# Kernel optimization log

Measured on AMD Instinct MI355X. Metric: run time of the kernel, lower is better.

Reference implementation:

```python
import jax, jax.numpy as jnp
import numpy as np

H = 8  # num_heads


def _ln(x, g, b):
    mu = x.mean(-1, keepdims=True)
    var = ((x - mu) ** 2).mean(-1, keepdims=True)
    return (x - mu) * jax.lax.rsqrt(var + 1e-5) * g + b


def setup_inputs() -> dict:
    key = jax.random.key(0)
    ks = jax.random.split(key, 24)
    B, N, V, E, D, R, L = 8, 512, 50000, 300, 256, 100, 4
    dh = D // H
    s = 0.02
    inp = {}
    inp['token_ids'] = jax.random.randint(ks[0], (B, N), 0, V, dtype=jnp.int32)
    inp['relations'] = jax.random.randint(ks[1], (B, N, N), 0, R, dtype=jnp.int32)
    m = jax.random.bernoulli(ks[2], 0.9, (B, N, N))
    eye = jnp.eye(N, dtype=bool)[None]
    inp['relations_mask'] = jnp.logical_or(m, eye)  # keep diagonal valid so every row attends somewhere
    inp['embed'] = jax.random.normal(ks[3], (V, E), jnp.float32) * s
    inp['W_in'] = jax.random.normal(ks[4], (E, D), jnp.float32) * s
    inp['b_in'] = jnp.zeros((D,), jnp.float32)
    inp['Wq'] = jax.random.normal(ks[5], (L, D, D), jnp.float32) * s
    inp['Wk'] = jax.random.normal(ks[6], (L, D, D), jnp.float32) * s
    inp['Wv'] = jax.random.normal(ks[7], (L, D, D), jnp.float32) * s
    inp['Wo'] = jax.random.normal(ks[8], (L, D, D), jnp.float32) * s
    inp['ln1_g'] = jnp.ones((L, D), jnp.float32)
    inp['ln1_b'] = jnp.zeros((L, D), jnp.float32)
    inp['ln2_g'] = jnp.ones((L, D), jnp.float32)
    inp['ln2_b'] = jnp.zeros((L, D), jnp.float32)
    inp['W1'] = jax.random.normal(ks[9], (L, D, 4 * D), jnp.float32) * s
    inp['b1'] = jnp.zeros((L, 4 * D), jnp.float32)
    inp['W2'] = jax.random.normal(ks[10], (L, 4 * D, D), jnp.float32) * s
    inp['b2'] = jnp.zeros((L, D), jnp.float32)
    inp['rel_k_emb'] = jax.random.normal(ks[11], (R, dh), jnp.float32) * s
    inp['rel_v_emb'] = jax.random.normal(ks[12], (R, dh), jnp.float32) * s
    inp['W_out'] = jax.random.normal(ks[13], (D, D), jnp.float32) * s
    inp['b_out'] = jnp.zeros((D,), jnp.float32)
    return inp


def reference(token_ids, relations, relations_mask, embed, W_in, b_in, Wq, Wk, Wv, Wo,
              ln1_g, ln1_b, ln2_g, ln2_b, W1, b1, W2, b2, rel_k_emb, rel_v_emb, W_out, b_out):
    # Input layer: embedding lookup + projection to gnn hidden size.
    x = embed[token_ids]                          # [B,N,E]
    x = jax.nn.relu(x @ W_in + b_in)              # [B,N,D]
    B, N, D = x.shape
    dh = D // H
    # Shared relation embeddings (share_layers=True, share_heads=True): gathered once.
    rk = rel_k_emb[relations]                     # [B,N,N,dh]
    rv = rel_v_emb[relations]                     # [B,N,N,dh]
    neg = jnp.asarray(-1e9, x.dtype)
    scale = jnp.asarray(1.0 / np.sqrt(dh), x.dtype)
    L = Wq.shape[0]
    for l in range(L):  # fixed small layer count
        q = (x @ Wq[l]).reshape(B, N, H, dh).transpose(0, 2, 1, 3)
        k = (x @ Wk[l]).reshape(B, N, H, dh).transpose(0, 2, 1, 3)
        v = (x @ Wv[l]).reshape(B, N, H, dh).transpose(0, 2, 1, 3)
        # Relation-aware scores: q.k + q.r_k (RAT-SQL)
        scores = (jnp.einsum('bhnd,bhmd->bhnm', q, k)
                  + jnp.einsum('bhnd,bnmd->bhnm', q, rk)) * scale
        scores = jnp.where(relations_mask[:, None], scores, neg)
        a = jax.nn.softmax(scores, axis=-1)       # [B,H,N,N]
        z = (jnp.einsum('bhnm,bhmd->bhnd', a, v)
             + jnp.einsum('bhnm,bnmd->bhnd', a, rv))
        z = z.transpose(0, 2, 1, 3).reshape(B, N, D) @ Wo[l]
        x = _ln(x + z, ln1_g[l], ln1_b[l])
        f = jax.nn.relu(x @ W1[l] + b1[l]) @ W2[l] + b2[l]
        x = _ln(x + f, ln2_g[l], ln2_b[l])
    # Output layer projection
    return x @ W_out + b_out
```

## Files before the change

### kernel.cpp

```cpp
#include <hip/hip_runtime.h>
#include <hip/hip_bf16.h>

#define NTOK 4096
#define NN   512

typedef __attribute__((ext_vector_type(8))) short bf16x8;
typedef __attribute__((ext_vector_type(4))) float f32x4;
typedef __attribute__((ext_vector_type(4))) unsigned short u16x4;

__device__ __forceinline__ float bf16_to_f(unsigned short u) {
    unsigned int x = ((unsigned int)u) << 16;
    return __builtin_bit_cast(float, x);
}
__device__ __forceinline__ unsigned short f_to_bf16(float f) {
    unsigned int b = __builtin_bit_cast(unsigned int, f);
    return (unsigned short)((b + 0x7fff + ((b >> 16) & 1)) >> 16);
}
__device__ __forceinline__ bf16x8 pack8(float4 a, float4 b) {
    bf16x8 v;
    v[0]=(short)f_to_bf16(a.x); v[1]=(short)f_to_bf16(a.y);
    v[2]=(short)f_to_bf16(a.z); v[3]=(short)f_to_bf16(a.w);
    v[4]=(short)f_to_bf16(b.x); v[5]=(short)f_to_bf16(b.y);
    v[6]=(short)f_to_bf16(b.z); v[7]=(short)f_to_bf16(b.w);
    return v;
}

__global__ void detect_mask_kernel(const unsigned char* __restrict__ m, int* __restrict__ flag) {
    __shared__ int f;
    if (threadIdx.x == 0) f = 0;
    __syncthreads();
    int any = 0;
    for (int i = threadIdx.x; i < 4096; i += 256) {
        if ((i & 3) != 0 && m[i] != 0) any = 1;
    }
    if (any) atomicOr(&f, 1);
    __syncthreads();
    if (threadIdx.x == 0) *flag = f;
}

__global__ __launch_bounds__(256) void prep_rel16(
    const int* __restrict__ rel, const void* __restrict__ mask,
    const int* __restrict__ flag, short* __restrict__ rel16)
{
    const bool mbyte = (*flag != 0);
    const unsigned char* m8 = (const unsigned char*)mask;
    const int* m32 = (const int*)mask;
    const int i = (blockIdx.x * 256 + threadIdx.x) * 2;
    int2 rv = *(const int2*)(rel + i);
    int ok0, ok1;
    if (mbyte) { ok0 = m8[i]; ok1 = m8[i + 1]; }
    else       { ok0 = (m32[i] != 0); ok1 = (m32[i + 1] != 0); }
    short2 o;
    o.x = ok0 ? (short)rv.x : (short)-1;
    o.y = ok1 ? (short)rv.y : (short)-1;
    *(short2*)(rel16 + i) = o;
}

__global__ __launch_bounds__(256) void tcast256(
    const float* __restrict__ Wq, const float* __restrict__ Wk,
    const float* __restrict__ Wv, const float* __restrict__ Wo,
    const float* __restrict__ Wout, unsigned short* __restrict__ wt,
    int nL, float scale)
{
    const int z = blockIdx.z;
    const float* src; unsigned short* dst; float sc = 1.f;
    if (z >= nL * 4) {
        src = Wout; dst = wt + (size_t)nL * 786432;
    } else {
        const int l = z >> 2, which = z & 3;
        if      (which == 0) { src = Wq + (size_t)l * 65536; sc = scale; }
        else if (which == 1) { src = Wk + (size_t)l * 65536; }
        else if (which == 2) { src = Wv + (size_t)l * 65536; }
        else                 { src = Wo + (size_t)l * 65536; }
        dst = wt + (size_t)l * 786432 + which * 65536;
    }
    __shared__ float tile[32][33];
    const int t = threadIdx.x, tx = t & 31, ty = t >> 5;
    const int n0 = blockIdx.x * 32, k0 = blockIdx.y * 32;
#pragma unroll
    for (int p = 0; p < 4; ++p)
        tile[ty + p * 8][tx] = src[(size_t)(k0 + ty + p * 8) * 256 + n0 + tx];
    __syncthreads();
#pragma unroll
    for (int p = 0; p < 4; ++p)
        dst[(size_t)(n0 + ty + p * 8) * 256 + k0 + tx] = f_to_bf16(tile[tx][ty + p * 8] * sc);
}

__global__ __launch_bounds__(256) void tcastKN(
    const float* __restrict__ in, unsigned short* __restrict__ out,
    int K, int N, long inStride, long outStride)
{
    in  += (size_t)blockIdx.z * inStride;
    out += (size_t)blockIdx.z * outStride;
    __shared__ float tile[32][33];
    const int t = threadIdx.x, tx = t & 31, ty = t >> 5;
    const int n0 = blockIdx.x * 32, k0 = blockIdx.y * 32;
#pragma unroll
    for (int p = 0; p < 4; ++p)
        tile[ty + p * 8][tx] = in[(size_t)(k0 + ty + p * 8) * N + n0 + tx];
    __syncthreads();
#pragma unroll
    for (int p = 0; p < 4; ++p)
        out[(size_t)(n0 + ty + p * 8) * K + k0 + tx] = f_to_bf16(tile[tx][ty + p * 8]);
}

__global__ __launch_bounds__(256) void embed_proj_kernel(
    const int* __restrict__ tok, const float* __restrict__ embed,
    const float* __restrict__ W_in, const float* __restrict__ b_in,
    float* __restrict__ x, unsigned short* __restrict__ xh)
{
    __shared__ float emb[8][304];
    __shared__ int tloc[8];
    const int t = threadIdx.x;
    const int r0 = blockIdx.x * 8;
    if (t < 8) tloc[t] = tok[r0 + t];
    __syncthreads();
    for (int i = t; i < 8 * 300; i += 256) {
        int r = i / 300, e = i - r * 300;
        emb[r][e] = embed[(size_t)tloc[r] * 300 + e];
    }
    __syncthreads();
    float acc[8] = {0.f,0.f,0.f,0.f,0.f,0.f,0.f,0.f};
    const int d = t;
    for (int e = 0; e < 300; ++e) {
        float w = W_in[e * 256 + d];
#pragma unroll
        for (int r = 0; r < 8; ++r) acc[r] += emb[r][e] * w;
    }
    const float bb = b_in[d];
#pragma unroll
    for (int r = 0; r < 8; ++r) {
        float o = acc[r] + bb;
        o = o > 0.f ? o : 0.f;
        x[(size_t)(r0 + r) * 256 + d] = o;
        xh[(size_t)(r0 + r) * 256 + d] = f_to_bf16(o);
    }
}

__global__ __launch_bounds__(256) void gemm_bf16_64(
    const unsigned short* __restrict__ A, const unsigned short* __restrict__ WT,
    const float* __restrict__ bias, float* __restrict__ Cf, unsigned short* __restrict__ Ch,
    int M, int K, int Nc, int relu)
{
    __shared__ unsigned short As[2][64][40];
    __shared__ unsigned short Bs[2][64][40];
    const int t = threadIdx.x;
    const int lane = t & 63, w = t >> 6;
    const int g = lane >> 4, li = lane & 15;
    const int r0 = blockIdx.y * 64, c0 = blockIdx.x * 64;

    f32x4 acc[4];
#pragma unroll
    for (int i = 0; i < 4; ++i) acc[i] = (f32x4){0.f,0.f,0.f,0.f};

    const int arow = t >> 2, ad8 = (t & 3) * 8;

    bf16x8 a0 = *(const bf16x8*)(A  + (size_t)(r0 + arow) * K + ad8);
    bf16x8 b0 = *(const bf16x8*)(WT + (size_t)(c0 + arow) * K + ad8);

    const int nk = K >> 5;
    for (int ki = 0; ki < nk; ++ki) {
        const int cur = ki & 1;
        *(bf16x8*)&As[cur][arow][ad8] = a0;
        *(bf16x8*)&Bs[cur][arow][ad8] = b0;
        if (ki + 1 < nk) {
            const int k0 = (ki + 1) * 32;
            a0 = *(const bf16x8*)(A  + (size_t)(r0 + arow) * K + k0 + ad8);
            b0 = *(const bf16x8*)(WT + (size_t)(c0 + arow) * K + k0 + ad8);
        }
        __syncthreads();
        bf16x8 af = *(const bf16x8*)&As[cur][16 * w + li][g * 8];
#pragma unroll
        for (int sub = 0; sub < 4; ++sub) {
            bf16x8 bfr = *(const bf16x8*)&Bs[cur][16 * sub + li][g * 8];
            acc[sub] = __builtin_amdgcn_mfma_f32_16x16x32_bf16(af, bfr, acc[sub], 0, 0, 0);
        }
    }
#pragma unroll
    for (int sub = 0; sub < 4; ++sub) {
        int col = c0 + sub * 16 + li;
        float bv = bias ? bias[col] : 0.f;
#pragma unroll
        for (int r = 0; r < 4; ++r) {
            int row = r0 + 16 * w + g * 4 + r;
            float o = acc[sub][r] + bv;
            if (relu) o = fmaxf(o, 0.f);
            if (Ch) Ch[(size_t)row * Nc + col] = f_to_bf16(o);
            else    Cf[(size_t)row * Nc + col] = o;
        }
    }
}

__global__ __launch_bounds__(256) void gemm_bf16_32(
    const unsigned short* __restrict__ A, const unsigned short* __restrict__ WT,
    const float* __restrict__ bias, float* __restrict__ Cf, unsigned short* __restrict__ Ch,
    int M, int K, int Nc, int relu)
{
    __shared__ unsigned short As[2][32][40];
    __shared__ unsigned short Bs[2][64][40];
    const int t = threadIdx.x;
    const int lane = t & 63, w = t >> 6;
    const int g = lane >> 4, li = lane & 15;
    const int r0 = blockIdx.y * 32, c0 = blockIdx.x * 64;

    f32x4 acc[2];
    acc[0] = (f32x4){0.f,0.f,0.f,0.f};
    acc[1] = (f32x4){0.f,0.f,0.f,0.f};

    const int arow = t >> 3, a4 = (t & 7) * 4;
    const int bcol = t >> 2, bk8 = (t & 3) * 8;

    u16x4 a0 = *(const u16x4*)(A + (size_t)(r0 + arow) * K + a4);
    bf16x8 b0 = *(const bf16x8*)(WT + (size_t)(c0 + bcol) * K + bk8);

    const int nk = K >> 5;
    for (int ki = 0; ki < nk; ++ki) {
        const int cur = ki & 1;
        *(u16x4*)&As[cur][arow][a4] = a0;
        *(bf16x8*)&Bs[cur][bcol][bk8] = b0;
        if (ki + 1 < nk) {
            const int k0 = (ki + 1) * 32;
            a0 = *(const u16x4*)(A + (size_t)(r0 + arow) * K + k0 + a4);
            b0 = *(const bf16x8*)(WT + (size_t)(c0 + bcol) * K + k0 + bk8);
        }
        __syncthreads();
        bf16x8 af = *(const bf16x8*)&As[cur][16 * (w & 1) + li][g * 8];
#pragma unroll
        for (int sub = 0; sub < 2; ++sub) {
            bf16x8 bfr = *(const bf16x8*)&Bs[cur][(w >> 1) * 32 + sub * 16 + li][g * 8];
            acc[sub] = __builtin_amdgcn_mfma_f32_16x16x32_bf16(af, bfr, acc[sub], 0, 0, 0);
        }
    }
#pragma unroll
    for (int sub = 0; sub < 2; ++sub) {
        int col = c0 + (w >> 1) * 32 + sub * 16 + li;
        float bv = bias ? bias[col] : 0.f;
#pragma unroll
        for (int r = 0; r < 4; ++r) {
            int row = r0 + 16 * (w & 1) + g * 4 + r;
            float o = acc[sub][r] + bv;
            if (relu) o = fmaxf(o, 0.f);
            if (Ch) Ch[(size_t)row * Nc + col] = f_to_bf16(o);
            else    Cf[(size_t)row * Nc + col] = o;
        }
    }
}

__global__ __launch_bounds__(256) void gemm_wo(
    const float* __restrict__ zpart, const float* __restrict__ smpart,
    const unsigned short* __restrict__ WT, float* __restrict__ Cf, int Nc)
{
    __shared__ unsigned short As[32][256];
    __shared__ unsigned short Bs[64][256];
    __shared__ float den[32][8];
    char* Ab = (char*)As; char* Bb = (char*)Bs;
    const int t = threadIdx.x;
    const int lane = t & 63, w = t >> 6;
    const int g = lane >> 4, li = lane & 15;
    const int r0 = blockIdx.y * 32, c0 = blockIdx.x * 64;

    {
        int row = t >> 3, h2 = t & 7;
        float s = smpart[(size_t)(r0 + row) * 8 + h2] +
                  smpart[32768 + (size_t)(r0 + row) * 8 + h2];
        den[row][h2] = 1.f / s;
    }
    __syncthreads();
#pragma unroll
    for (int j = 0; j < 4; ++j) {
        int idx = j * 256 + t;
        int row = idx >> 5;
        int k8 = (idx & 31) * 8;
        const float* z0 = zpart + (size_t)(r0 + row) * 256 + k8;
        const float* z1 = z0 + 1048576;
        float4 a0 = *(const float4*)z0, a1 = *(const float4*)(z0 + 4);
        float4 b0 = *(const float4*)z1, b1 = *(const float4*)(z1 + 4);
        float dv = den[row][k8 >> 5];
        a0.x = (a0.x + b0.x) * dv; a0.y = (a0.y + b0.y) * dv;
        a0.z = (a0.z + b0.z) * dv; a0.w = (a0.w + b0.w) * dv;
        a1.x = (a1.x + b1.x) * dv; a1.y = (a1.y + b1.y) * dv;
        a1.z = (a1.z + b1.z) * dv; a1.w = (a1.w + b1.w) * dv;
        int colb = (idx & 31) * 16;
        int sw = row * 512 + (colb ^ ((row & 7) << 4));
        *(bf16x8*)(Ab + sw) = pack8(a0, a1);
    }
#pragma unroll
    for (int j = 0; j < 8; ++j) {
        int idx = j * 256 + t;
        int row = idx >> 5;
        int colb = (idx & 31) * 16;
        int sw = row * 512 + (colb ^ ((row & 7) << 4));
        *(bf16x8*)(Bb + sw) = *(const bf16x8*)(WT + (size_t)(c0 + row) * 256 + (idx & 31) * 8);
    }
    __syncthreads();
    f32x4 acc[2];
    acc[0] = (f32x4){0.f,0.f,0.f,0.f};
    acc[1] = (f32x4){0.f,0.f,0.f,0.f};
    const int arow = 16 * (w & 1) + li;
    const int xr = (li & 7) << 4;
#pragma unroll
    for (int ks = 0; ks < 8; ++ks) {
        const int kb = (g * 8 + ks * 32) * 2;
        bf16x8 af = *(const bf16x8*)(Ab + arow * 512 + (kb ^ xr));
#pragma unroll
        for (int sub = 0; sub < 2; ++sub) {
            const int brow = (w >> 1) * 32 + sub * 16 + li;
            bf16x8 bfr = *(const bf16x8*)(Bb + brow * 512 + (kb ^ xr));
            acc[sub] = __builtin_amdgcn_mfma_f32_16x16x32_bf16(af, bfr, acc[sub], 0, 0, 0);
        }
    }
#pragma unroll
    for (int sub = 0; sub < 2; ++sub) {
        int col = c0 + (w >> 1) * 32 + sub * 16 + li;
#pragma unroll
        for (int r = 0; r < 4; ++r) {
            int row = r0 + 16 * (w & 1) + g * 4 + r;
            Cf[(size_t)row * Nc + col] = acc[sub][r];
        }
    }
}

__global__ __launch_bounds__(256) void qrk_kernel(
    const unsigned short* __restrict__ qkvh, const float* __restrict__ relk_g,
    unsigned short* __restrict__ qrkg)
{
    const int n0 = blockIdx.x * 64, h = blockIdx.y, b = blockIdx.z;
    const int t = threadIdx.x, lane = t & 63, w = t >> 6;
    const int g = lane >> 4, li = lane & 15;
    const int qrow = 16 * w + g * 4;

    __shared__ unsigned short relk_s[100][40];
    for (int i = t; i < 400; i += 256) {
        int rr = i >> 2, d8 = (i & 3) * 8;
        const float* sp = relk_g + rr * 32 + d8;
        *(bf16x8*)&relk_s[rr][d8] = pack8(*(const float4*)sp, *(const float4*)(sp + 4));
    }
    bf16x8 qf = *(const bf16x8*)(qkvh + (size_t)(b * NN + n0 + 16 * w + li) * 768 + h * 32 + g * 8);
    __syncthreads();
#pragma unroll
    for (int rc = 0; rc < 7; ++rc) {
        bf16x8 bb = *(const bf16x8*)&relk_s[rc * 16 + li][g * 8];
        f32x4 s = __builtin_amdgcn_mfma_f32_16x16x32_bf16(qf, bb, (f32x4){0.f,0.f,0.f,0.f}, 0, 0, 0);
        int col = rc * 16 + li;
        if (col < 100) {
#pragma unroll
            for (int r = 0; r < 4; ++r)
                qrkg[((size_t)(b * 8 + h) * NN + n0 + qrow + r) * 100 + col] = f_to_bf16(s[r]);
        }
    }
}

__global__ __launch_bounds__(256, 4) void attn_mfma(
    const unsigned short* __restrict__ qkvh,
    const short* __restrict__ rel16,
    const unsigned short* __restrict__ qrkg,
    const float* __restrict__ relv_g,
    float* __restrict__ zpart, float* __restrict__ smpart)
{
    const int p = blockIdx.x;
    const int cx = p & 7, k = p >> 3;
    const int sg = cx * 16 + (k >> 3);
    const int h  = k & 7;
    const int b = sg >> 4, chunk = sg & 15;
    const int n0 = chunk * 32;

    const int t = threadIdx.x;
    const int lane = t & 63, w = t >> 6;
    const int qw = w & 1, mhalf = w >> 1;
    const int g = lane >> 4, li = lane & 15;
    const int qrow = 16 * qw + g * 4;
    const int mbase = mhalf * 256;

    __shared__ float wrel[32][100];
    __shared__ unsigned short qrk_lds[32][100];
    __shared__ union {
        unsigned short relvT[32][136];
        struct {
            unsigned short v_t[2][2][32][40];
            unsigned short p_s[4][16][40];
        } mn;
    } u;

    for (int i = t; i < 3200; i += 256) ((float*)wrel)[i] = 0.f;
    {
        const unsigned short* qsrc = qrkg + ((size_t)(b * 8 + h) * NN + n0) * 100;
        for (int i = t; i < 1600; i += 256) {
            int row = i / 50, off = (i - row * 50) * 2;
            *(unsigned int*)&qrk_lds[row][off] =
                *(const unsigned int*)(qsrc + (size_t)row * 100 + off);
        }
    }
    bf16x8 qf = *(const bf16x8*)(qkvh + (size_t)(b * NN + n0 + 16 * qw + li) * 768 + h * 32 + g * 8);

    const short* relrow[4];
#pragma unroll
    for (int r = 0; r < 4; ++r)
        relrow[r] = rel16 + ((size_t)b * NN + n0 + qrow + r) * NN;
    const int th = t & 127;
    const int vm = th & 31, vdg = th >> 5;
    const size_t kRB = (size_t)(b * NN) * 768 + 256 + h * 32 + g * 8;
    const size_t vRB = (size_t)(b * NN) * 768 + 512 + h * 32 + vdg * 8;

    bf16x8 kbuf[2][2]; bf16x8 vbuf[2]; short rbuf[2][8];
#pragma unroll
    for (int i = 0; i < 8; ++i)
        rbuf[0][i] = relrow[i & 3][mbase + (i >> 2) * 16 + li];
    kbuf[0][0] = *(const bf16x8*)(qkvh + kRB + (size_t)(mbase + li) * 768);
    kbuf[0][1] = *(const bf16x8*)(qkvh + kRB + (size_t)(mbase + 16 + li) * 768);
    vbuf[0]    = *(const bf16x8*)(qkvh + vRB + (size_t)(mbase + vm) * 768);

    float smacc[4] = {0.f, 0.f, 0.f, 0.f};
    f32x4 zf[2];
    zf[0] = (f32x4){0.f,0.f,0.f,0.f};
    zf[1] = (f32x4){0.f,0.f,0.f,0.f};

#pragma unroll
    for (int tt = 0; tt < 8; ++tt) {
        const int cur = tt & 1, nxt = cur ^ 1;
        {
            bf16x8 vv = vbuf[cur];
#pragma unroll
            for (int j = 0; j < 8; ++j)
                u.mn.v_t[mhalf][cur][vdg * 8 + j][vm] = (unsigned short)vv[j];
        }
        if (tt + 1 < 8) {
            const int m0n = mbase + (tt + 1) * 32;
#pragma unroll
            for (int i = 0; i < 8; ++i)
                rbuf[nxt][i] = relrow[i & 3][m0n + (i >> 2) * 16 + li];
        }
        __syncthreads();
        bf16x8 kf0 = kbuf[cur][0], kf1 = kbuf[cur][1];
        if (tt + 1 < 8) {
            const int m0n = mbase + (tt + 1) * 32;
            kbuf[nxt][0] = *(const bf16x8*)(qkvh + kRB + (size_t)(m0n + li) * 768);
            kbuf[nxt][1] = *(const bf16x8*)(qkvh + kRB + (size_t)(m0n + 16 + li) * 768);
            vbuf[nxt]    = *(const bf16x8*)(qkvh + vRB + (size_t)(m0n + vm) * 768);
        }
        f32x4 s0 = __builtin_amdgcn_mfma_f32_16x16x32_bf16(qf, kf0, (f32x4){0.f,0.f,0.f,0.f}, 0, 0, 0);
        f32x4 s1 = __builtin_amdgcn_mfma_f32_16x16x32_bf16(qf, kf1, (f32x4){0.f,0.f,0.f,0.f}, 0, 0, 0);
        float pr[8];
#pragma unroll
        for (int i = 0; i < 8; ++i) {
            const int r = i & 3;
            const int rl = rbuf[cur][i];
            const float qadd = bf16_to_f(qrk_lds[qrow + r][rl < 0 ? 0 : rl]);
            const float sv = ((i >> 2) ? s1[r] : s0[r]) + qadd;
            float pv = 0.f;
            if (rl >= 0) {
                pv = __expf(fminf(sv, 50.f));
                atomicAdd(&wrel[qrow + r][rl], pv);
            }
            smacc[r] += pv;
            pr[i] = pv;
        }
#pragma unroll
        for (int i = 0; i < 8; ++i)
            u.mn.p_s[w][g * 4 + (i & 3)][(i >> 2) * 16 + li] = f_to_bf16(pr[i]);
        asm volatile("s_waitcnt lgkmcnt(0)" ::: "memory");
        __builtin_amdgcn_sched_barrier(0);
        bf16x8 pa = *(const bf16x8*)&u.mn.p_s[w][li][g * 8];
#pragma unroll
        for (int dc = 0; dc < 2; ++dc) {
            bf16x8 vb = *(const bf16x8*)&u.mn.v_t[mhalf][cur][dc * 16 + li][g * 8];
            zf[dc] = __builtin_amdgcn_mfma_f32_16x16x32_bf16(pa, vb, zf[dc], 0, 0, 0);
        }
    }
    __syncthreads();

    for (int i = t; i < 32 * 36; i += 256) {
        int d = i / 36, c = 100 + (i - (i / 36) * 36);
        u.relvT[d][c] = 0;
    }
    for (int i = t; i < 400; i += 256) {
        int rr2 = i >> 2, d8 = (i & 3) * 8;
        const float* sp = relv_g + rr2 * 32 + d8;
        float4 s0 = *(const float4*)sp, s1 = *(const float4*)(sp + 4);
        u.relvT[d8 + 0][rr2] = f_to_bf16(s0.x);
        u.relvT[d8 + 1][rr2] = f_to_bf16(s0.y);
        u.relvT[d8 + 2][rr2] = f_to_bf16(s0.z);
        u.relvT[d8 + 3][rr2] = f_to_bf16(s0.w);
        u.relvT[d8 + 4][rr2] = f_to_bf16(s1.x);
        u.relvT[d8 + 5][rr2] = f_to_bf16(s1.y);
        u.relvT[d8 + 6][rr2] = f_to_bf16(s1.z);
        u.relvT[d8 + 7][rr2] = f_to_bf16(s1.w);
    }
    __syncthreads();
    if (mhalf == 0) {
#pragma unroll
        for (int kc = 0; kc < 4; ++kc) {
            const int kbase = kc * 32 + g * 8;
            const float* wp = &wrel[16 * qw + li][0];
            bf16x8 af;
#pragma unroll
            for (int j = 0; j < 8; ++j) {
                int id = kbase + j;
                float val = (id < 100) ? wp[id] : 0.f;
                af[j] = (short)f_to_bf16(val);
            }
#pragma unroll
            for (int dc = 0; dc < 2; ++dc) {
                bf16x8 vbr = *(const bf16x8*)&u.relvT[dc * 16 + li][kbase];
                zf[dc] = __builtin_amdgcn_mfma_f32_16x16x32_bf16(af, vbr, zf[dc], 0, 0, 0);
            }
        }
    }
#pragma unroll
    for (int r = 0; r < 4; ++r) {
        smacc[r] += __shfl_xor(smacc[r], 1, 64);
        smacc[r] += __shfl_xor(smacc[r], 2, 64);
        smacc[r] += __shfl_xor(smacc[r], 4, 64);
        smacc[r] += __shfl_xor(smacc[r], 8, 64);
    }
#pragma unroll
    for (int r = 0; r < 4; ++r) {
        const int row = b * NN + n0 + qrow + r;
        size_t ob = (size_t)mhalf * 1048576 + (size_t)row * 256 + h * 32;
#pragma unroll
        for (int dc = 0; dc < 2; ++dc)
            zpart[ob + dc * 16 + li] = zf[dc][r];
        if (li == 0)
            smpart[(size_t)mhalf * 32768 + (size_t)row * 8 + h] = smacc[r];
    }
}

__global__ __launch_bounds__(256) void ln_kernel(
    const float* __restrict__ xin, const float* __restrict__ y,
    const float* __restrict__ g, const float* __restrict__ bsh,
    float* __restrict__ xout, unsigned short* __restrict__ xh)
{
    const int t = threadIdx.x;
    const int w = t >> 6, lane = t & 63;
    const size_t row = (size_t)blockIdx.x * 4 + w;
    const float4 xv = *(const float4*)(xin + row * 256 + lane * 4);
    const float4 yv = *(const float4*)(y + row * 256 + lane * 4);
    float4 sv;
    sv.x = xv.x + yv.x; sv.y = xv.y + yv.y; sv.z = xv.z + yv.z; sv.w = xv.w + yv.w;
    float sum = sv.x + sv.y + sv.z + sv.w;
    float sq  = sv.x * sv.x + sv.y * sv.y + sv.z * sv.z + sv.w * sv.w;
#pragma unroll
    for (int off = 1; off < 64; off <<= 1) {
        sum += __shfl_xor(sum, off, 64);
        sq  += __shfl_xor(sq, off, 64);
    }
    const float mu = sum * (1.f / 256.f);
    const float var = sq * (1.f / 256.f) - mu * mu;
    const float rs = rsqrtf(var + 1e-5f);
    const float4 gv = *(const float4*)(g + lane * 4);
    const float4 bv = *(const float4*)(bsh + lane * 4);
    float4 o;
    o.x = (sv.x - mu) * rs * gv.x + bv.x;
    o.y = (sv.y - mu) * rs * gv.y + bv.y;
    o.z = (sv.z - mu) * rs * gv.z + bv.z;
    o.w = (sv.w - mu) * rs * gv.w + bv.w;
    *(float4*)(xout + row * 256 + lane * 4) = o;
    u16x4 oh;
    oh[0] = f_to_bf16(o.x); oh[1] = f_to_bf16(o.y);
    oh[2] = f_to_bf16(o.z); oh[3] = f_to_bf16(o.w);
    *(u16x4*)(xh + row * 256 + lane * 4) = oh;
}

extern "C" void kernel_launch(void* const* d_in, const int* in_sizes, int n_in,
                              void* d_out, int out_size, void* d_ws, size_t ws_size,
                              hipStream_t stream)
{
    (void)in_sizes; (void)n_in; (void)out_size;
    const int*   tok   = (const int*)d_in[0];
    const int*   rel   = (const int*)d_in[1];
    const void*  mask  = d_in[2];
    const float* embed = (const float*)d_in[3];
    const float* W_in  = (const float*)d_in[4];
    const float* b_in  = (const float*)d_in[5];
    const float* Wq    = (const float*)d_in[6];
    const float* Wk    = (const float*)d_in[7];
    const float* Wv    = (const float*)d_in[8];
    const float* Wo    = (const float*)d_in[9];
    const float* ln1g  = (const float*)d_in[10];
    const float* ln1b  = (const float*)d_in[11];
    const float* ln2g  = (const float*)d_in[12];
    const float* ln2b  = (const float*)d_in[13];
    const float* W1    = (const float*)d_in[14];
    const float* b1    = (const float*)d_in[15];
    const float* W2    = (const float*)d_in[16];
    const float* b2    = (const float*)d_in[17];
    const float* relk  = (const float*)d_in[18];
    const float* relv  = (const float*)d_in[19];
    const float* Wout  = (const float*)d_in[20];
    const float* bout  = (const float*)d_in[21];
    float* out = (float*)d_out;
    const float scale = 0.17677669529663687f;

    float* ws = (float*)d_ws;
    float*          x     = ws;
    unsigned short* xh    = (unsigned short*)(ws + 1048576);
    float*          zo    = ws + 2097152;
    unsigned short* qkvh  = (unsigned short*)(ws + 3145728);
    unsigned short* hbh   = (unsigned short*)(ws + 4718592);
    float*          zpart = ws + 6815744;
    float*          smpart= ws + 8912896;
    unsigned short* qrkg  = (unsigned short*)(ws + 8978432);
    int*            flag  = (int*)(ws + 10616832);
    unsigned short* wt    = (unsigned short*)(ws + 10616848);

    const size_t wsf = ws_size >> 2;
    const bool tierA = wsf >= 13271100;
    short* rel16 = tierA ? (short*)(ws + 12222480) : (short*)hbh;

    detect_mask_kernel<<<1, 256, 0, stream>>>((const unsigned char*)mask, flag);
    embed_proj_kernel<<<512, 256, 0, stream>>>(tok, embed, W_in, b_in, x, xh);
    if (tierA) {
        prep_rel16<<<4096, 256, 0, stream>>>(rel, mask, flag, rel16);
        tcast256<<<dim3(8, 8, 17), 256, 0, stream>>>(Wq, Wk, Wv, Wo, Wout, wt, 4, scale);
        tcastKN<<<dim3(32, 8, 4), 256, 0, stream>>>(W1, wt + 262144, 256, 1024, 262144, 786432);
        tcastKN<<<dim3(8, 32, 4), 256, 0, stream>>>(W2, wt + 524288, 1024, 256, 262144, 786432);
    }

    for (int l = 0; l < 4; ++l) {
        unsigned short* wl = tierA ? wt + (size_t)l * 786432 : wt;
        if (!tierA) {
            prep_rel16<<<4096, 256, 0, stream>>>(rel, mask, flag, rel16);
            tcast256<<<dim3(8, 8, 4), 256, 0, stream>>>(
                Wq + (size_t)l * 65536, Wk + (size_t)l * 65536,
                Wv + (size_t)l * 65536, Wo + (size_t)l * 65536, Wout, wt, 1, scale);
            tcastKN<<<dim3(32, 8, 1), 256, 0, stream>>>(W1 + (size_t)l * 262144, wt + 262144, 256, 1024, 0, 0);
            tcastKN<<<dim3(8, 32, 1), 256, 0, stream>>>(W2 + (size_t)l * 262144, wt + 524288, 1024, 256, 0, 0);
        }
        gemm_bf16_64<<<dim3(12, 64), 256, 0, stream>>>(xh, wl, nullptr, nullptr, qkvh,
                                                       NTOK, 256, 768, 0);
        qrk_kernel<<<dim3(8, 8, 8), 256, 0, stream>>>(qkvh, relk, qrkg);
        attn_mfma<<<1024, 256, 0, stream>>>(qkvh, rel16, qrkg, relv, zpart, smpart);
        gemm_wo<<<dim3(4, 128), 256, 0, stream>>>(zpart, smpart, wl + 196608, zo, 256);
        ln_kernel<<<1024, 256, 0, stream>>>(x, zo, ln1g + l * 256, ln1b + l * 256, x, xh);
        gemm_bf16_64<<<dim3(16, 64), 256, 0, stream>>>(xh, wl + 262144, b1 + l * 1024, nullptr, hbh,
                                                       NTOK, 256, 1024, 1);
        gemm_bf16_32<<<dim3(4, 128), 256, 0, stream>>>(hbh, wl + 524288, b2 + l * 256, zo, nullptr,
                                                       NTOK, 1024, 256, 0);
        ln_kernel<<<1024, 256, 0, stream>>>(x, zo, ln2g + l * 256, ln2b + l * 256, x, xh);
    }
    unsigned short* woutT = wt;
    if (tierA) {
        woutT = wt + (size_t)4 * 786432;
    } else {
        tcast256<<<dim3(8, 8, 1), 256, 0, stream>>>(Wq, Wk, Wv, Wo, Wout, wt, 0, scale);
    }
    gemm_bf16_32<<<dim3(4, 128), 256, 0, stream>>>(xh, woutT, bout, out, nullptr,
                                                   NTOK, 256, 256, 0);
}
```

Measured before the change: 619.9 us.

## Split attention key range into four partitions with 512-thread blocks

The attention kernel now runs 512 threads per block, with four wave-pairs each covering a quarter of the key range instead of two covering halves. Each pass therefore does 4 key tiles instead of 8. The output projection kernel reduces four partial z and softmax-denominator slices instead of two. The workspace is re-laid out so zpart aliases the FFN hidden buffer, and the tier threshold changes to match. This adds more waves per block to hide latency, at the cost of twice the partial-sum traffic, an extra barrier per iteration now that the V staging buffer is single-buffered, and possible register pressure from the tighter launch bounds.

```diff
diff --git a/kernel.cpp b/kernel.cpp
--- a/kernel.cpp
+++ b/kernel.cpp
@@ -261,8 +261,10 @@
 
     {
         int row = t >> 3, h2 = t & 7;
-        float s = smpart[(size_t)(r0 + row) * 8 + h2] +
-                  smpart[32768 + (size_t)(r0 + row) * 8 + h2];
+        float s = 0.f;
+#pragma unroll
+        for (int sl = 0; sl < 4; ++sl)
+            s += smpart[(size_t)sl * 32768 + (size_t)(r0 + row) * 8 + h2];
         den[row][h2] = 1.f / s;
     }
     __syncthreads();
@@ -272,14 +274,17 @@
         int row = idx >> 5;
         int k8 = (idx & 31) * 8;
         const float* z0 = zpart + (size_t)(r0 + row) * 256 + k8;
-        const float* z1 = z0 + 1048576;
         float4 a0 = *(const float4*)z0, a1 = *(const float4*)(z0 + 4);
-        float4 b0 = *(const float4*)z1, b1 = *(const float4*)(z1 + 4);
+#pragma unroll
+        for (int sl = 1; sl < 4; ++sl) {
+            const float* zs = z0 + (size_t)sl * 1048576;
+            float4 b0 = *(const float4*)zs, b1 = *(const float4*)(zs + 4);
+            a0.x += b0.x; a0.y += b0.y; a0.z += b0.z; a0.w += b0.w;
+            a1.x += b1.x; a1.y += b1.y; a1.z += b1.z; a1.w += b1.w;
+        }
         float dv = den[row][k8 >> 5];
-        a0.x = (a0.x + b0.x) * dv; a0.y = (a0.y + b0.y) * dv;
-        a0.z = (a0.z + b0.z) * dv; a0.w = (a0.w + b0.w) * dv;
-        a1.x = (a1.x + b1.x) * dv; a1.y = (a1.y + b1.y) * dv;
-        a1.z = (a1.z + b1.z) * dv; a1.w = (a1.w + b1.w) * dv;
+        a0.x *= dv; a0.y *= dv; a0.z *= dv; a0.w *= dv;
+        a1.x *= dv; a1.y *= dv; a1.z *= dv; a1.w *= dv;
         int colb = (idx & 31) * 16;
         int sw = row * 512 + (colb ^ ((row & 7) << 4));
         *(bf16x8*)(Ab + sw) = pack8(a0, a1);
@@ -350,12 +355,13 @@
     }
 }
 
-__global__ __launch_bounds__(256, 4) void attn_mfma(
+__global__ __launch_bounds__(512, 8) void attn_mfma(
     const unsigned short* __restrict__ qkvh,
     const short* __restrict__ rel16,
     const unsigned short* __restrict__ qrkg,
     const float* __restrict__ relv_g,
-    float* __restrict__ zpart, float* __restrict__ smpart)
+    float* __restrict__ zpart,
+    float* __restrict__ smpart)
 {
     const int p = blockIdx.x;
     const int cx = p & 7, k = p >> 3;
@@ -366,25 +372,25 @@
 
     const int t = threadIdx.x;
     const int lane = t & 63, w = t >> 6;
-    const int qw = w & 1, mhalf = w >> 1;
+    const int qw = w & 1, mq = w >> 1;
     const int g = lane >> 4, li = lane & 15;
     const int qrow = 16 * qw + g * 4;
-    const int mbase = mhalf * 256;
+    const int mbase = mq * 128;
 
     __shared__ float wrel[32][100];
     __shared__ unsigned short qrk_lds[32][100];
     __shared__ union {
         unsigned short relvT[32][136];
         struct {
-            unsigned short v_t[2][2][32][40];
-            unsigned short p_s[4][16][40];
+            unsigned short v_t[4][32][40];
+            unsigned short p_s[8][16][40];
         } mn;
     } u;
 
-    for (int i = t; i < 3200; i += 256) ((float*)wrel)[i] = 0.f;
+    for (int i = t; i < 3200; i += 512) ((float*)wrel)[i] = 0.f;
     {
         const unsigned short* qsrc = qrkg + ((size_t)(b * 8 + h) * NN + n0) * 100;
-        for (int i = t; i < 1600; i += 256) {
+        for (int i = t; i < 1600; i += 512) {
             int row = i / 50, off = (i - row * 50) * 2;
             *(unsigned int*)&qrk_lds[row][off] =
                 *(const unsigned int*)(qsrc + (size_t)row * 100 + off);
@@ -415,15 +421,15 @@
     zf[1] = (f32x4){0.f,0.f,0.f,0.f};
 
 #pragma unroll
-    for (int tt = 0; tt < 8; ++tt) {
+    for (int tt = 0; tt < 4; ++tt) {
         const int cur = tt & 1, nxt = cur ^ 1;
         {
             bf16x8 vv = vbuf[cur];
 #pragma unroll
             for (int j = 0; j < 8; ++j)
-                u.mn.v_t[mhalf][cur][vdg * 8 + j][vm] = (unsigned short)vv[j];
-        }
-        if (tt + 1 < 8) {
+                u.mn.v_t[mq][vdg * 8 + j][vm] = (unsigned short)vv[j];
+        }
+        if (tt + 1 < 4) {
             const int m0n = mbase + (tt + 1) * 32;
 #pragma unroll
             for (int i = 0; i < 8; ++i)
@@ -431,7 +437,7 @@
         }
         __syncthreads();
         bf16x8 kf0 = kbuf[cur][0], kf1 = kbuf[cur][1];
-        if (tt + 1 < 8) {
+        if (tt + 1 < 4) {
             const int m0n = mbase + (tt + 1) * 32;
             kbuf[nxt][0] = *(const bf16x8*)(qkvh + kRB + (size_t)(m0n + li) * 768);
             kbuf[nxt][1] = *(const bf16x8*)(qkvh + kRB + (size_t)(m0n + 16 + li) * 768);
@@ -462,17 +468,17 @@
         bf16x8 pa = *(const bf16x8*)&u.mn.p_s[w][li][g * 8];
 #pragma unroll
         for (int dc = 0; dc < 2; ++dc) {
-            bf16x8 vb = *(const bf16x8*)&u.mn.v_t[mhalf][cur][dc * 16 + li][g * 8];
+            bf16x8 vb = *(const bf16x8*)&u.mn.v_t[mq][dc * 16 + li][g * 8];
             zf[dc] = __builtin_amdgcn_mfma_f32_16x16x32_bf16(pa, vb, zf[dc], 0, 0, 0);
         }
-    }
-    __syncthreads();
-
-    for (int i = t; i < 32 * 36; i += 256) {
+        __syncthreads();
+    }
+
+    for (int i = t; i < 32 * 36; i += 512) {
         int d = i / 36, c = 100 + (i - (i / 36) * 36);
         u.relvT[d][c] = 0;
     }
-    for (int i = t; i < 400; i += 256) {
+    for (int i = t; i < 400; i += 512) {
         int rr2 = i >> 2, d8 = (i & 3) * 8;
         const float* sp = relv_g + rr2 * 32 + d8;
         float4 s0 = *(const float4*)sp, s1 = *(const float4*)(sp + 4);
@@ -486,7 +492,7 @@
         u.relvT[d8 + 7][rr2] = f_to_bf16(s1.w);
     }
     __syncthreads();
-    if (mhalf == 0) {
+    if (mq == 0) {
 #pragma unroll
         for (int kc = 0; kc < 4; ++kc) {
             const int kbase = kc * 32 + g * 8;
@@ -515,12 +521,12 @@
 #pragma unroll
     for (int r = 0; r < 4; ++r) {
         const int row = b * NN + n0 + qrow + r;
-        size_t ob = (size_t)mhalf * 1048576 + (size_t)row * 256 + h * 32;
+        size_t ob = (size_t)mq * 1048576 + (size_t)row * 256 + h * 32;
 #pragma unroll
         for (int dc = 0; dc < 2; ++dc)
             zpart[ob + dc * 16 + li] = zf[dc][r];
         if (li == 0)
-            smpart[(size_t)mhalf * 32768 + (size_t)row * 8 + h] = smacc[r];
+            smpart[(size_t)mq * 32768 + (size_t)row * 8 + h] = smacc[r];
     }
 }
 
@@ -593,18 +599,18 @@
     float* ws = (float*)d_ws;
     float*          x     = ws;
     unsigned short* xh    = (unsigned short*)(ws + 1048576);
-    float*          zo    = ws + 2097152;
-    unsigned short* qkvh  = (unsigned short*)(ws + 3145728);
-    unsigned short* hbh   = (unsigned short*)(ws + 4718592);
-    float*          zpart = ws + 6815744;
-    float*          smpart= ws + 8912896;
-    unsigned short* qrkg  = (unsigned short*)(ws + 8978432);
-    int*            flag  = (int*)(ws + 10616832);
-    unsigned short* wt    = (unsigned short*)(ws + 10616848);
+    float*          zo    = ws + 1572864;
+    unsigned short* qkvh  = (unsigned short*)(ws + 2621440);
+    float*          zpart = ws + 4194304;
+    unsigned short* hbh   = (unsigned short*)(ws + 4194304);
+    float*          smpart= ws + 8388608;
+    unsigned short* qrkg  = (unsigned short*)(ws + 8519680);
+    int*            flag  = (int*)(ws + 10158080);
+    unsigned short* wt    = (unsigned short*)(ws + 10158096);
 
     const size_t wsf = ws_size >> 2;
-    const bool tierA = wsf >= 13271100;
-    short* rel16 = tierA ? (short*)(ws + 12222480) : (short*)hbh;
+    const bool tierA = wsf >= 13860700;
+    short* rel16 = tierA ? (short*)(ws + 11763728) : (short*)zo;
 
     detect_mask_kernel<<<1, 256, 0, stream>>>((const unsigned char*)mask, flag);
     embed_proj_kernel<<<512, 256, 0, stream>>>(tok, embed, W_in, b_in, x, xh);
@@ -628,7 +634,7 @@
         gemm_bf16_64<<<dim3(12, 64), 256, 0, stream>>>(xh, wl, nullptr, nullptr, qkvh,
                                                        NTOK, 256, 768, 0);
         qrk_kernel<<<dim3(8, 8, 8), 256, 0, stream>>>(qkvh, relk, qrkg);
-        attn_mfma<<<1024, 256, 0, stream>>>(qkvh, rel16, qrkg, relv, zpart, smpart);
+        attn_mfma<<<1024, 512, 0, stream>>>(qkvh, rel16, qrkg, relv, zpart, smpart);
         gemm_wo<<<dim3(4, 128), 256, 0, stream>>>(zpart, smpart, wl + 196608, zo, 256);
         ln_kernel<<<1024, 256, 0, stream>>>(x, zo, ln1g + l * 256, ln1b + l * 256, x, xh);
         gemm_bf16_64<<<dim3(16, 64), 256, 0, stream>>>(xh, wl + 262144, b1 + l * 1024, nullptr, hbh,
```

Measured after the change: 673.2 us. 8.6% more time.
